# Kernel tuning notes

Measured on AMD Instinct MI355X. Metric: run time of the kernel, lower is better.

Reference implementation:

```python
import jax, jax.numpy as jnp
import numpy as np
from jax import lax

GAMMA = 0.01
BIG = 1e8  # stand-in for +inf on DP borders (keeps grads finite/zero)


def _pairwise_sq_dists(x, y):
    # x: [N,1] (target), y: [N,1] (pred) -> D[i,j] = (x_i - y_j)^2
    xn = jnp.sum(x * x, axis=1)  # [N]
    yn = jnp.sum(y * y, axis=1)  # [N]
    d = xn[:, None] + yn[None, :] - 2.0 * (x @ y.T)
    return jnp.maximum(d, 0.0)


def _soft_dtw(D, gamma):
    # Soft-DTW DP via wavefront scan over the 2N-1 anti-diagonals.
    # R[i,j] = D[i,j] + softmin_gamma(R[i-1,j-1], R[i-1,j], R[i,j-1]),
    # with virtual R[-1,-1] = 0 and +inf borders.
    N = D.shape[0]
    ii = jnp.arange(N)

    def shift(r):  # r[i] -> r[i-1], BIG at i=0
        return jnp.concatenate([jnp.full((1,), BIG, r.dtype), r[:-1]])

    def step(carry, k):
        r1, r2 = carry  # diagonals k-1 and k-2, indexed by row i
        jj = k - ii
        valid = (jj >= 0) & (jj < N)
        d = D[ii, jnp.clip(jj, 0, N - 1)]
        a = shift(r2)                                   # R[i-1, j-1]
        a = jnp.where((k == 0) & (ii == 0), 0.0, a)     # virtual origin
        b = shift(r1)                                   # R[i-1, j]
        c = jnp.where(jj >= 1, r1, BIG)                 # R[i, j-1]
        vals = jnp.stack([a, b, c])                     # [3, N]
        m = jnp.min(vals, axis=0)
        softmin = m - gamma * jnp.log(jnp.sum(jnp.exp(-(vals - m) / gamma), axis=0))
        r_new = jnp.where(valid, d + softmin, BIG)
        return (r_new, r1), None

    init = jnp.full((N,), BIG, D.dtype)
    (r_last, _), _ = lax.scan(step, (init, init), jnp.arange(2 * N - 1))
    return r_last[N - 1]  # R[N-1, N-1], batch size 1 -> mean == value


def setup_inputs() -> dict:
    key = jax.random.key(0)
    k1, k2 = jax.random.split(key)
    pred = jax.random.normal(k1, (4096, 1), dtype=jnp.float32)
    target = jax.random.normal(k2, (4096, 1), dtype=jnp.float32)
    return {"pred": pred, "target": target}


def reference(pred, target):
    # DILATELoss.forward returns loss_shape (the soft-DTW value);
    # the temporal path term is computed in the original but discarded.
    D = _pairwise_sq_dists(target.reshape(-1, 1), pred.reshape(-1, 1))
    return _soft_dtw(D, GAMMA)
```

## Files before the change

### kernel.cpp

```cpp
#include <hip/hip_runtime.h>

#define NN    4096
#define BIGF  1e8f
#define SQK2f 12.0112245225638540f
#define BIGK  1.4426950408889634e10f
#define IK2f  0.00693147180559945309f
#define NBLK  32
#define NCI   132
#define OUTS  4222
#define SENTU 0xFFFFFFFFu

__global__ __launch_bounds__(1024) void dilate_sdtw(const float* __restrict__ pred,
                                                    const float* __restrict__ target,
                                                    float* __restrict__ out) {
    __shared__ float t_s[NN];
    __shared__ float p_s[NN];
    __shared__ float bufA[NN];
    __shared__ float bufB[NN];
    __shared__ float bufC[NN];
    const int tid = threadIdx.x;
    for (int i = tid; i < NN; i += 1024) {
        t_s[i] = target[i]; p_s[i] = pred[i];
        bufA[i] = BIGF; bufB[i] = BIGF; bufC[i] = BIGF;
    }
    __syncthreads();
    float* r2 = bufA; float* r1 = bufB; float* rn = bufC;
    for (int k = 0; k < 2 * NN - 1; ++k) {
        int ilo = k - (NN - 1); if (ilo < 0) ilo = 0;
        int ihi = (k < NN - 1) ? k : (NN - 1);
        for (int i = ilo + tid; i <= ihi; i += 1024) {
            const int j = k - i;
            float diff = t_s[i] - p_s[j];
            float d = diff * diff;
            float a = (i >= 1 && j >= 1) ? r2[i - 1] : ((k == 0) ? 0.0f : BIGF);
            float b = (i >= 1) ? r1[i - 1] : BIGF;
            float c = (j >= 1) ? r1[i] : BIGF;
            float m = fminf(a, fminf(b, c));
            float s = __expf((m - a) * 100.0f) + __expf((m - b) * 100.0f) + __expf((m - c) * 100.0f);
            rn[i] = d + m - 0.01f * __logf(s);
        }
        __syncthreads();
        float* tmp = r2; r2 = r1; r1 = rn; rn = tmp;
    }
    if (tid == 0) out[0] = r1[NN - 1];
}


__device__ __forceinline__ float softmin3s(float a, float b, float c) {
    float m = fminf(a, fminf(b, c));
    float e = __builtin_amdgcn_exp2f(m - a)
            + __builtin_amdgcn_exp2f(m - b)
            + __builtin_amdgcn_exp2f(m - c);
    return m - __builtin_amdgcn_logf(e);
}

__device__ __forceinline__ float nbr1(float v, bool bsel) {
    int iv = __float_as_int(v);
    float a = __int_as_float(__builtin_amdgcn_update_dpp(iv, iv, 0x111, 0xF, 0xF, false));
    float b = __int_as_float(__builtin_amdgcn_update_dpp(iv, iv, 0x142, 0xF, 0xF, false));
    return bsel ? b : a;
}

__device__ __forceinline__ void bput(float* p, float v) {
    __hip_atomic_store((unsigned int*)p, __float_as_uint(v),
                       __ATOMIC_RELAXED, __HIP_MEMORY_SCOPE_AGENT);
}
__device__ __forceinline__ unsigned int bgetu(const float* p) {
    return __hip_atomic_load((const unsigned int*)p,
                             __ATOMIC_RELAXED, __HIP_MEMORY_SCOPE_AGENT);
}

__device__ __forceinline__ void uissue(const float* src, float* dst) {
#pragma unroll
    for (int q = 0; q < 32; ++q) dst[q] = __uint_as_float(bgetu(src + q));
}
__device__ __forceinline__ bool uvalid(const float* dst) {
    bool ok = true;
#pragma unroll
    for (int q = 0; q < 32; ++q) ok &= (__float_as_uint(dst[q]) != SENTU);
    return ok;
}
__device__ __forceinline__ void upoll(const float* src, float* dst) {
    for (;;) {
        uissue(src, dst);
        if (uvalid(dst)) return;
        __builtin_amdgcn_s_sleep(1);
    }
}

__device__ __forceinline__ void pload(const float* p_s, int base, float* dst) {
#pragma unroll
    for (int q = 0; q < 33; ++q) {
        int idx = base + q;
        idx = idx < 0 ? 0 : (idx > NN - 1 ? NN - 1 : idx);
        dst[q] = p_s[idx];
    }
}

template<bool TOP, bool BOT, bool EDGE>
__device__ __forceinline__ void chunk32(
    int cs, int lane, bool l0, bool bsel, float t0, float t1,
    float& v0p, float& v0pp, float& v1p, float& u1, float& u2, float upl,
    float4& acc, const float* upc, const float* pc,
    float* __restrict__ bnd_my, float* __restrict__ outp)
{
#pragma unroll
    for (int u = 0; u < 32; ++u) {
        const int s  = cs + u;
        const int j0 = s - 2 * lane;
        const int j1 = j0 - 1;
        float a0, b0;
        if (TOP) {
            a0 = l0 ? ((s == 0) ? 0.0f : BIGK) : u2;
            b0 = l0 ? BIGK : u1;
        } else {
            float upj  = upc[u];
            float upjm = (u == 0) ? upl : upc[u - 1];
            a0 = l0 ? upjm : u2;
            b0 = l0 ? upj  : u1;
        }
        float d0 = t0 - pc[u + 1];
        float val0 = fmaf(d0, d0, softmin3s(a0, b0, v0p));
        float d1 = t1 - pc[u];
        float val1 = fmaf(d1, d1, softmin3s(v0pp, v0p, v1p));
        if (EDGE) {
            val0 = ((unsigned)j0 < (unsigned)NN) ? val0 : BIGK;
            val1 = ((unsigned)j1 < (unsigned)NN) ? val1 : BIGK;
        }
        if (!BOT) {
            switch ((u + 1) & 3) {
                case 0: acc.x = val1; break;
                case 1: acc.y = val1; break;
                case 2: acc.z = val1; break;
                case 3: acc.w = val1; break;
            }
            if ((u & 3) == 2) {
                int base = j1 - 3;
                if (lane == 63 && (!EDGE || (unsigned)base <= (unsigned)(NN - 4))) {
                    bput(bnd_my + base + 0, acc.x);
                    bput(bnd_my + base + 1, acc.y);
                    bput(bnd_my + base + 2, acc.z);
                    bput(bnd_my + base + 3, acc.w);
                }
            }
        } else if (EDGE) {
            if (lane == 63 && s == OUTS) outp[0] = val1 * IK2f;
        }
        v0pp = v0p; v0p = val0; v1p = val1;
        u2 = u1;
        u1 = nbr1(val1, bsel);
    }
}

template<bool TOP, bool BOT>
__device__ __forceinline__ void chunk_iter(
    int ci, int lane, bool l0, bool bsel, float t0, float t1,
    float& v0p, float& v0pp, float& v1p, float& u1, float& u2, float& upl,
    float4& acc,
    float* upC, float* upN, float* pcC, float* pcN,
    const float* p_s, const float* __restrict__ bnd_up, float* __restrict__ bnd_my,
    float* __restrict__ outp)
{
    const int cs = 32 * ci;
    if (!TOP && cs < NN) {
        if (!uvalid(upC)) upoll(bnd_up + cs, upC);
        if (cs + 32 < NN) uissue(bnd_up + cs + 32, upN);
    }
    if (ci + 1 < NCI) pload(p_s, cs + 32 - 1 - 2 * lane, pcN);

    const bool edge = (ci < 4) || (ci >= 128);
    if (edge) chunk32<TOP, BOT, true >(cs, lane, l0, bsel, t0, t1, v0p, v0pp, v1p,
                                       u1, u2, upl, acc, upC, pcC, bnd_my, outp);
    else      chunk32<TOP, BOT, false>(cs, lane, l0, bsel, t0, t1, v0p, v0pp, v1p,
                                       u1, u2, upl, acc, upC, pcC, bnd_my, outp);
    if (!TOP) upl = upC[31];
}

template<bool TOP, bool BOT>
__device__ void stripe(int b, int lane, const float* __restrict__ target,
                       const float* p_s, float* bnd, float* outp)
{
    const float t0 = target[128 * b + 2 * lane]     * SQK2f;
    const float t1 = target[128 * b + 2 * lane + 1] * SQK2f;
    float* bnd_my = bnd + (size_t)b * NN;
    const float* bnd_up = bnd + (size_t)(b - 1) * NN;
    const bool l0 = (lane == 0);
    const bool bsel = (lane != 0) && ((lane & 15) == 0);

    float v0p = BIGK, v0pp = BIGK, v1p = BIGK, u1 = BIGK, u2 = BIGK, upl = BIGK;
    float4 acc = {BIGK, BIGK, BIGK, BIGK};
    float upA[32], upB[32];
    float pcA[33], pcB[33];

    pload(p_s, -1 - 2 * lane, pcA);
    if (!TOP) uissue(bnd_up, upA);

    for (int cp = 0; cp < NCI / 2; ++cp) {
        chunk_iter<TOP, BOT>(2 * cp,     lane, l0, bsel, t0, t1, v0p, v0pp, v1p, u1, u2, upl, acc,
                             upA, upB, pcA, pcB, p_s, bnd_up, bnd_my, outp);
        chunk_iter<TOP, BOT>(2 * cp + 1, lane, l0, bsel, t0, t1, v0p, v0pp, v1p, u1, u2, upl, acc,
                             upB, upA, pcB, pcA, p_s, bnd_up, bnd_my, outp);
    }
}

__global__ __launch_bounds__(64, 1) void sdtw_pipe10(const float* __restrict__ pred,
                                                     const float* __restrict__ target,
                                                     float* __restrict__ out,
                                                     float* __restrict__ bnd)
{
    __shared__ float p_s[NN];
    const int lane = threadIdx.x;
    const int bid = blockIdx.x;
    const int b = (bid & 7) * 4 + (bid >> 3);
    for (int i = lane; i < NN; i += 64) p_s[i] = pred[i] * SQK2f;
    __syncthreads();
    if (b == 0)                stripe<true , false>(b, lane, target, p_s, bnd, out);
    else if (b == NBLK - 1)    stripe<false, true >(b, lane, target, p_s, bnd, out);
    else                       stripe<false, false>(b, lane, target, p_s, bnd, out);
}

extern "C" void kernel_launch(void* const* d_in, const int* in_sizes, int n_in,
                              void* d_out, int out_size, void* d_ws, size_t ws_size,
                              hipStream_t stream) {
    const float* pred   = (const float*)d_in[0];
    const float* target = (const float*)d_in[1];
    float* out = (float*)d_out;

    const size_t need = (size_t)NBLK * NN * sizeof(float);
    if (ws_size >= need) {
        float* bnd = (float*)d_ws;
        hipMemsetAsync(d_ws, 0xFF, need, stream);
        sdtw_pipe10<<<dim3(NBLK), dim3(64), 0, stream>>>(pred, target, out, bnd);
    } else {
        dilate_sdtw<<<dim3(1), dim3(1024), 0, stream>>>(pred, target, out);
    }
}
```

Measured before the change: 1.035 ms.

## Compute 2x2 cell tiles per lane step to halve wavefront steps

```diff
diff --git a/kernel.cpp b/kernel.cpp
--- a/kernel.cpp
+++ b/kernel.cpp
@@ -6,8 +6,9 @@
 #define BIGK  1.4426950408889634e10f
 #define IK2f  0.00693147180559945309f
 #define NBLK  32
+#define SCH   16
 #define NCI   132
-#define OUTS  4222
+#define OUTS  2110
 #define SENTU 0xFFFFFFFFu
 
 __global__ __launch_bounds__(1024) void dilate_sdtw(const float* __restrict__ pred,
@@ -88,76 +89,87 @@
     }
 }
 
-__device__ __forceinline__ void pload(const float* p_s, int base, float* dst) {
-#pragma unroll
-    for (int q = 0; q < 33; ++q) {
-        int idx = base + q;
-        idx = idx < 0 ? 0 : (idx > NN - 1 ? NN - 1 : idx);
-        dst[q] = p_s[idx];
+__device__ __forceinline__ void pload(const float* p_s, int base, float2* dst) {
+#pragma unroll
+    for (int q = 0; q < 16; ++q) {
+        int idx = base + 2 * q;
+        idx = idx < 0 ? 0 : (idx > NN - 2 ? NN - 2 : idx);
+        dst[q] = *(const float2*)(p_s + idx);
     }
 }
 
 template<bool TOP, bool BOT, bool EDGE>
-__device__ __forceinline__ void chunk32(
-    int cs, int lane, bool l0, bool bsel, float t0, float t1,
-    float& v0p, float& v0pp, float& v1p, float& u1, float& u2, float upl,
-    float4& acc, const float* upc, const float* pc,
+__device__ __forceinline__ void chunkC2(
+    int ci, int lane, bool l0, bool bsel, float t0, float t1,
+    float& v0b, float& v1b, float& u1a, float& u1b, float& u2b, float upl,
+    float2& acc, const float* upc, const float2* pc,
     float* __restrict__ bnd_my, float* __restrict__ outp)
 {
 #pragma unroll
-    for (int u = 0; u < 32; ++u) {
-        const int s  = cs + u;
-        const int j0 = s - 2 * lane;
-        const int j1 = j0 - 1;
-        float a0, b0;
+    for (int u = 0; u < SCH; ++u) {
+        const int s  = SCH * ci + u;
+        const int jA = 2 * s - 2 * lane;
+        float aA, bA, bB;
         if (TOP) {
-            a0 = l0 ? ((s == 0) ? 0.0f : BIGK) : u2;
-            b0 = l0 ? BIGK : u1;
+            aA = l0 ? ((s == 0) ? 0.0f : BIGK) : u2b;
+            bA = l0 ? BIGK : u1a;
+            bB = l0 ? BIGK : u1b;
         } else {
-            float upj  = upc[u];
-            float upjm = (u == 0) ? upl : upc[u - 1];
-            a0 = l0 ? upjm : u2;
-            b0 = l0 ? upj  : u1;
-        }
-        float d0 = t0 - pc[u + 1];
-        float val0 = fmaf(d0, d0, softmin3s(a0, b0, v0p));
-        float d1 = t1 - pc[u];
-        float val1 = fmaf(d1, d1, softmin3s(v0pp, v0p, v1p));
+            float upjm = (u == 0) ? upl : upc[2 * u - 1];
+            aA = l0 ? upjm         : u2b;
+            bA = l0 ? upc[2 * u]     : u1a;
+            bB = l0 ? upc[2 * u + 1] : u1b;
+        }
+        float2 pj = pc[u];
+        float dA0 = t0 - pj.x;
+        float val0a = fmaf(dA0, dA0, softmin3s(aA, bA, v0b));
+        float dB0 = t0 - pj.y;
+        float val0b = fmaf(dB0, dB0, softmin3s(bA, bB, val0a));
+        float dA1 = t1 - pj.x;
+        float val1a = fmaf(dA1, dA1, softmin3s(v0b, val0a, v1b));
+        float dB1 = t1 - pj.y;
+        float val1b_ = fmaf(dB1, dB1, softmin3s(val0a, val0b, val1a));
         if (EDGE) {
-            val0 = ((unsigned)j0 < (unsigned)NN) ? val0 : BIGK;
-            val1 = ((unsigned)j1 < (unsigned)NN) ? val1 : BIGK;
+            bool vA = (unsigned)jA < (unsigned)NN;
+            bool vB = (unsigned)(jA + 1) < (unsigned)NN;
+            val0a = vA ? val0a : BIGK;  val1a  = vA ? val1a  : BIGK;
+            val0b = vB ? val0b : BIGK;  val1b_ = vB ? val1b_ : BIGK;
         }
         if (!BOT) {
-            switch ((u + 1) & 3) {
-                case 0: acc.x = val1; break;
-                case 1: acc.y = val1; break;
-                case 2: acc.z = val1; break;
-                case 3: acc.w = val1; break;
-            }
-            if ((u & 3) == 2) {
-                int base = j1 - 3;
-                if (lane == 63 && (!EDGE || (unsigned)base <= (unsigned)(NN - 4))) {
-                    bput(bnd_my + base + 0, acc.x);
-                    bput(bnd_my + base + 1, acc.y);
-                    bput(bnd_my + base + 2, acc.z);
-                    bput(bnd_my + base + 3, acc.w);
+            if (EDGE) {
+                if (lane == 63) {
+                    if ((unsigned)jA < (unsigned)NN)       bput(bnd_my + jA,     val1a);
+                    if ((unsigned)(jA + 1) < (unsigned)NN) bput(bnd_my + jA + 1, val1b_);
+                }
+            } else {
+                if (u & 1) {
+                    if (lane == 63) {
+                        const int base = jA - 2;
+                        bput(bnd_my + base + 0, acc.x);
+                        bput(bnd_my + base + 1, acc.y);
+                        bput(bnd_my + base + 2, val1a);
+                        bput(bnd_my + base + 3, val1b_);
+                    }
+                } else {
+                    acc.x = val1a; acc.y = val1b_;
                 }
             }
         } else if (EDGE) {
-            if (lane == 63 && s == OUTS) outp[0] = val1 * IK2f;
-        }
-        v0pp = v0p; v0p = val0; v1p = val1;
-        u2 = u1;
-        u1 = nbr1(val1, bsel);
+            if (lane == 63 && s == OUTS) outp[0] = val1b_ * IK2f;
+        }
+        u2b = u1b;
+        u1a = nbr1(val1a,  bsel);
+        u1b = nbr1(val1b_, bsel);
+        v0b = val0b; v1b = val1b_;
     }
 }
 
 template<bool TOP, bool BOT>
 __device__ __forceinline__ void chunk_iter(
     int ci, int lane, bool l0, bool bsel, float t0, float t1,
-    float& v0p, float& v0pp, float& v1p, float& u1, float& u2, float& upl,
-    float4& acc,
-    float* upC, float* upN, float* pcC, float* pcN,
+    float& v0b, float& v1b, float& u1a, float& u1b, float& u2b, float& upl,
+    float2& acc,
+    float* upC, float* upN, float2* pcC, float2* pcN,
     const float* p_s, const float* __restrict__ bnd_up, float* __restrict__ bnd_my,
     float* __restrict__ outp)
 {
@@ -166,14 +178,14 @@
         if (!uvalid(upC)) upoll(bnd_up + cs, upC);
         if (cs + 32 < NN) uissue(bnd_up + cs + 32, upN);
     }
-    if (ci + 1 < NCI) pload(p_s, cs + 32 - 1 - 2 * lane, pcN);
+    if (ci + 1 < NCI) pload(p_s, cs + 32 - 2 * lane, pcN);
 
     const bool edge = (ci < 4) || (ci >= 128);
-    if (edge) chunk32<TOP, BOT, true >(cs, lane, l0, bsel, t0, t1, v0p, v0pp, v1p,
-                                       u1, u2, upl, acc, upC, pcC, bnd_my, outp);
-    else      chunk32<TOP, BOT, false>(cs, lane, l0, bsel, t0, t1, v0p, v0pp, v1p,
-                                       u1, u2, upl, acc, upC, pcC, bnd_my, outp);
-    if (!TOP) upl = upC[31];
+    if (edge) chunkC2<TOP, BOT, true >(ci, lane, l0, bsel, t0, t1, v0b, v1b,
+                                       u1a, u1b, u2b, upl, acc, upC, pcC, bnd_my, outp);
+    else      chunkC2<TOP, BOT, false>(ci, lane, l0, bsel, t0, t1, v0b, v1b,
+                                       u1a, u1b, u2b, upl, acc, upC, pcC, bnd_my, outp);
+    if (!TOP && cs < NN) upl = upC[31];
 }
 
 template<bool TOP, bool BOT>
@@ -187,26 +199,28 @@
     const bool l0 = (lane == 0);
     const bool bsel = (lane != 0) && ((lane & 15) == 0);
 
-    float v0p = BIGK, v0pp = BIGK, v1p = BIGK, u1 = BIGK, u2 = BIGK, upl = BIGK;
-    float4 acc = {BIGK, BIGK, BIGK, BIGK};
+    float v0b = BIGK, v1b = BIGK, u1a = BIGK, u1b = BIGK, u2b = BIGK, upl = BIGK;
+    float2 acc = {BIGK, BIGK};
     float upA[32], upB[32];
-    float pcA[33], pcB[33];
-
-    pload(p_s, -1 - 2 * lane, pcA);
+    float2 pcA[16], pcB[16];
+
+    pload(p_s, -2 * lane, pcA);
     if (!TOP) uissue(bnd_up, upA);
 
     for (int cp = 0; cp < NCI / 2; ++cp) {
-        chunk_iter<TOP, BOT>(2 * cp,     lane, l0, bsel, t0, t1, v0p, v0pp, v1p, u1, u2, upl, acc,
+        chunk_iter<TOP, BOT>(2 * cp,     lane, l0, bsel, t0, t1, v0b, v1b,
+                             u1a, u1b, u2b, upl, acc,
                              upA, upB, pcA, pcB, p_s, bnd_up, bnd_my, outp);
-        chunk_iter<TOP, BOT>(2 * cp + 1, lane, l0, bsel, t0, t1, v0p, v0pp, v1p, u1, u2, upl, acc,
+        chunk_iter<TOP, BOT>(2 * cp + 1, lane, l0, bsel, t0, t1, v0b, v1b,
+                             u1a, u1b, u2b, upl, acc,
                              upB, upA, pcB, pcA, p_s, bnd_up, bnd_my, outp);
     }
 }
 
-__global__ __launch_bounds__(64, 1) void sdtw_pipe10(const float* __restrict__ pred,
-                                                     const float* __restrict__ target,
-                                                     float* __restrict__ out,
-                                                     float* __restrict__ bnd)
+__global__ __launch_bounds__(64, 1) void sdtw_c2(const float* __restrict__ pred,
+                                                 const float* __restrict__ target,
+                                                 float* __restrict__ out,
+                                                 float* __restrict__ bnd)
 {
     __shared__ float p_s[NN];
     const int lane = threadIdx.x;
@@ -230,7 +244,7 @@
     if (ws_size >= need) {
         float* bnd = (float*)d_ws;
         hipMemsetAsync(d_ws, 0xFF, need, stream);
-        sdtw_pipe10<<<dim3(NBLK), dim3(64), 0, stream>>>(pred, target, out, bnd);
+        sdtw_c2<<<dim3(NBLK), dim3(64), 0, stream>>>(pred, target, out, bnd);
     } else {
         dilate_sdtw<<<dim3(1), dim3(1024), 0, stream>>>(pred, target, out);
     }
```

Result: slower. 1.139 ms (+10.0%).
